# Performance work log

Measured on AMD Instinct MI355X. Metric: run time of the kernel, lower is better.

The kernel has to match this reference:

```python
import jax, jax.numpy as jnp
import numpy as np

SCALE = 1.0 / (100.0 ** 0.5)  # module hard-codes QK / sqrt(100)


def setup_inputs() -> dict:
    key = jax.random.key(0)
    k1, k2, k3 = jax.random.split(key, 3)
    B, S, D = 8, 2048, 512
    head_size = 64
    x = jax.random.normal(k1, (B, S, D), dtype=jnp.float32)
    kernel = jax.random.normal(k2, (3, D, head_size), dtype=jnp.float32) * 0.02
    dense = jax.random.normal(k3, (D, D), dtype=jnp.float32) * 0.02
    return {"x": x, "kernel": kernel, "dense": dense, "heads": 8}


def reference(x, kernel, dense, heads):
    # All heads use the SAME kernel slices in the original loop, so each
    # iteration produces an identical V; compute once and tile.
    WQ = jnp.einsum('bsd,dh->bsh', x, kernel[0])  # [B,S,Hd]
    WK = jnp.einsum('bsd,dh->bsh', x, kernel[1])
    WV = jnp.einsum('bsd,dh->bsh', x, kernel[2])
    scores = jnp.einsum('bqh,bkh->bqk', WQ, WK) * SCALE  # [B,S,S]
    attn = jax.nn.softmax(scores, axis=-1)
    V = jnp.einsum('bqk,bkh->bqh', attn, WV)  # [B,S,Hd]
    out = jnp.tile(V, (1, 1, heads))  # concat of identical heads -> [B,S,heads*Hd]
    return jnp.einsum('bsf,fo->bso', out, dense)
```

## Files before the change

### kernel.cpp

```cpp
#include <hip/hip_runtime.h>
#include <math.h>


typedef __bf16 bf16;
typedef __bf16 bf16x4v __attribute__((ext_vector_type(4)));
typedef __bf16 bf16x8v __attribute__((ext_vector_type(8)));
typedef float f32x4 __attribute__((ext_vector_type(4)));

namespace {
constexpr int kS = 2048;
constexpr int kD = 512;
constexpr int kH = 64;
constexpr int kRows = 16384;
}

#define MFMA16(a, b, c) __builtin_amdgcn_mfma_f32_16x16x32_bf16((a), (b), (c), 0, 0, 0)

__global__ __launch_bounds__(256) void prep_kernel(const float* __restrict__ w,
                                                   const float* __restrict__ dense,
                                                   bf16* __restrict__ wtg,
                                                   float* __restrict__ dr) {
  int idx = blockIdx.x * 256 + threadIdx.x;
  if (idx < 98304) {
    int mat = idx >> 15, rem = idx & 32767;
    int n = rem >> 9, k = rem & 511;
    wtg[idx] = (bf16)w[mat * 32768 + k * 64 + n];
  } else {
    int e = idx - 98304;
    int j = e >> 9, o = e & 511;
    float s = 0.f;
#pragma unroll
    for (int h = 0; h < 8; ++h) s += dense[(size_t)(h * 64 + j) * kD + o];
    dr[e] = s;
  }
}

__global__ __launch_bounds__(256) void proj_kernel(const float* __restrict__ x,
                                                   const bf16* __restrict__ wtg,
                                                   bf16* __restrict__ wq,
                                                   bf16* __restrict__ wk,
                                                   bf16* __restrict__ wvt) {
  const int bt = blockIdx.x;
  const int tid = threadIdx.x;
  const int w = tid >> 6, tx = tid & 15, quad = (tid >> 4) & 3;
  const int row0 = bt * 64;

  __shared__ bf16 Xs[64 * 72];
  __shared__ bf16 Wts[3 * 64 * 72];

  f32x4 acc[3][4];
#pragma unroll
  for (int m = 0; m < 3; ++m)
#pragma unroll
    for (int nt = 0; nt < 4; ++nt) acc[m][nt] = (f32x4){0.f, 0.f, 0.f, 0.f};

  for (int k0 = 0; k0 < kD; k0 += 64) {
    __syncthreads();
#pragma unroll
    for (int p = 0; p < 4; ++p) {
      int i4 = tid + p * 256;
      int r = i4 >> 4, c4 = (i4 & 15) * 4;
      float4 f = *(const float4*)&x[(size_t)(row0 + r) * kD + k0 + c4];
      bf16x4v h = {(bf16)f.x, (bf16)f.y, (bf16)f.z, (bf16)f.w};
      *(bf16x4v*)&Xs[r * 72 + c4] = h;
    }
#pragma unroll
    for (int p = 0; p < 6; ++p) {
      int cc = tid + p * 256;
      int mat = cc >> 9, rem = cc & 511;
      int n = rem >> 3, c8 = (rem & 7) * 8;
      *(uint4*)&Wts[(mat * 64 + n) * 72 + c8] =
          *(const uint4*)&wtg[(size_t)mat * 32768 + (size_t)n * 512 + k0 + c8];
    }
    __syncthreads();
#pragma unroll
    for (int s = 0; s < 2; ++s) {
      bf16x8v a = *(bf16x8v*)&Xs[(w * 16 + tx) * 72 + s * 32 + quad * 8];
#pragma unroll
      for (int m = 0; m < 3; ++m)
#pragma unroll
        for (int nt = 0; nt < 4; ++nt) {
          bf16x8v bfr =
              *(bf16x8v*)&Wts[(m * 64 + nt * 16 + tx) * 72 + s * 32 + quad * 8];
          acc[m][nt] = MFMA16(a, bfr, acc[m][nt]);
        }
    }
  }

#pragma unroll
  for (int nt = 0; nt < 4; ++nt)
#pragma unroll
    for (int r = 0; r < 4; ++r) {
      int row_g = row0 + w * 16 + quad * 4 + r;
      int col = nt * 16 + tx;
      wq[(size_t)row_g * 64 + col] = (bf16)acc[0][nt][r];
      wk[(size_t)row_g * 64 + col] = (bf16)acc[1][nt][r];
    }
  __syncthreads();
  bf16* Vt = Xs;
#pragma unroll
  for (int nt = 0; nt < 4; ++nt)
#pragma unroll
    for (int r = 0; r < 4; ++r)
      Vt[(nt * 16 + tx) * 72 + (w * 16 + quad * 4 + r)] = (bf16)acc[2][nt][r];
  __syncthreads();
#pragma unroll
  for (int p = 0; p < 2; ++p) {
    int c = tid + p * 256;
    int v = c >> 3, seg = c & 7;
    *(uint4*)&wvt[(size_t)v * kRows + row0 + seg * 8] =
        *(uint4*)&Vt[v * 72 + seg * 8];
  }
}

__global__ __launch_bounds__(512, 4) void flash_kernel(
    const bf16* __restrict__ wq, const bf16* __restrict__ wk,
    const bf16* __restrict__ wvt, float* __restrict__ vo) {
  const int bid = blockIdx.x;
  const int b = bid & 7, qb = bid >> 3;
  const int q0 = qb * 32;
  const int tid = threadIdx.x;
  const int w = tid >> 6, lane = tid & 63, tx = tid & 15, quad = (tid >> 4) & 3;

  __shared__ __align__(16) char lds[65536];
  __shared__ float Lsh[256];
  bf16* Ksw = (bf16*)(lds + w * 8192);
  bf16* Psw = Ksw;
  bf16* Vtw = (bf16*)(lds + w * 8192 + 4096);

  const bf16* wqb = wq + (size_t)(b * kS) * 64;
  const bf16* wkb = wk + (size_t)(b * kS) * 64;
  const bf16* wvb = wvt + b * kS;

  const int kc0 = (quad ^ (tx & 7)) * 8;
  const int kc1 = ((4 + quad) ^ (tx & 7)) * 8;
  const int h2 = (tx ^ (tx >> 2)) & 3;

  bf16x8v aq[2][2];
#pragma unroll
  for (int rt = 0; rt < 2; ++rt)
#pragma unroll
    for (int s = 0; s < 2; ++s)
      aq[rt][s] = *(const bf16x8v*)&wqb[(size_t)(q0 + rt * 16 + tx) * 64 +
                                        s * 32 + quad * 8];

  f32x4 oacc[2][4];
#pragma unroll
  for (int rt = 0; rt < 2; ++rt)
#pragma unroll
    for (int nt = 0; nt < 4; ++nt) oacc[rt][nt] = (f32x4){0.f, 0.f, 0.f, 0.f};
  float lsum[2][4] = {};

  const int ksr = lane >> 3, kslc = lane & 7;
  const int vsv = lane >> 2, vsck = lane & 3;

  for (int t = 0; t < 8; ++t) {
    const int k0 = (t * 8 + w) * 32;
#pragma unroll
    for (int j = 0; j < 4; ++j) {
      int r = ksr + j * 8;
      *(uint4*)&Ksw[r * 64 + ((kslc ^ (r & 7)) * 8)] =
          *(const uint4*)&wkb[(size_t)(k0 + r) * 64 + kslc * 8];
      int v = vsv + j * 16;
      *(uint4*)&Vtw[v * 32 + ((vsck ^ ((v ^ (v >> 2)) & 3)) * 8)] =
          *(const uint4*)&wvb[(size_t)v * kRows + k0 + vsck * 8];
    }

#pragma unroll
    for (int nt = 0; nt < 2; ++nt) {
      int krow = nt * 16 + tx;
      bf16x8v b0 = *(bf16x8v*)&Ksw[krow * 64 + kc0];
      bf16x8v b1 = *(bf16x8v*)&Ksw[krow * 64 + kc1];
#pragma unroll
      for (int rt = 0; rt < 2; ++rt) {
        f32x4 z = (f32x4){0.f, 0.f, 0.f, 0.f};
        z = MFMA16(aq[rt][0], b0, z);
        z = MFMA16(aq[rt][1], b1, z);
#pragma unroll
        for (int r = 0; r < 4; ++r) {
          float p = __expf(z[r] * 0.1f);
          lsum[rt][r] += p;
          int q = rt * 16 + quad * 4 + r;
          int chunk = nt * 2 + (tx >> 3);
          Psw[q * 32 + ((chunk ^ (r ^ quad)) * 8) + (tx & 7)] = (bf16)p;
        }
      }
    }

#pragma unroll
    for (int rt = 0; rt < 2; ++rt) {
      bf16x8v pa = *(bf16x8v*)&Psw[(rt * 16 + tx) * 32 + ((quad ^ h2) * 8)];
#pragma unroll
      for (int nt = 0; nt < 4; ++nt) {
        bf16x8v vb = *(bf16x8v*)&Vtw[(nt * 16 + tx) * 32 + ((quad ^ h2) * 8)];
        oacc[rt][nt] = MFMA16(pa, vb, oacc[rt][nt]);
      }
    }
  }

  __syncthreads();
  float* myO = (float*)(lds + w * 8192);
  float* myL = Lsh + w * 32;
#pragma unroll
  for (int rt = 0; rt < 2; ++rt)
#pragma unroll
    for (int nt = 0; nt < 4; ++nt)
#pragma unroll
      for (int r = 0; r < 4; ++r)
        myO[(rt * 16 + quad * 4 + r) * 64 + nt * 16 + tx] = oacc[rt][nt][r];
#pragma unroll
  for (int rt = 0; rt < 2; ++rt)
#pragma unroll
    for (int r = 0; r < 4; ++r) {
      float v = lsum[rt][r];
#pragma unroll
      for (int m = 1; m < 16; m <<= 1) v += __shfl_xor(v, m, 64);
      if (tx == 0) myL[rt * 16 + quad * 4 + r] = v;
    }
  __syncthreads();

#pragma unroll
  for (int p = 0; p < 4; ++p) {
    int e = tid + p * 512;
    int row = e >> 6;
    float s = 0.f, lt = 0.f;
#pragma unroll
    for (int wv = 0; wv < 8; ++wv) {
      s += ((const float*)(lds + wv * 8192))[e];
      lt += Lsh[wv * 32 + row];
    }
    vo[(size_t)(b * kS + q0 + row) * 64 + (e & 63)] = s / lt;
  }
}

__global__ __launch_bounds__(256) void out_gemm_kernel(
    const float* __restrict__ v, const float* __restrict__ dr,
    float* __restrict__ out) {
  const int rt = blockIdx.x, ct = blockIdx.y;
  const int tid = threadIdx.x;
  const int tx = tid & 15, ty = tid >> 4;

  __shared__ float As[64][68];
  __shared__ float Bs[64][68];

#pragma unroll
  for (int p = 0; p < 4; ++p) {
    int f4 = tid + p * 256;
    int r = f4 >> 4, c = (f4 & 15) * 4;
    *(float4*)&As[r][c] = *(const float4*)(v + (size_t)(rt * 64 + r) * kH + c);
    *(float4*)&Bs[r][c] = *(const float4*)(dr + (size_t)r * kD + ct * 64 + c);
  }
  __syncthreads();

  float acc[4][4] = {};
#pragma unroll
  for (int k = 0; k < 64; k += 4) {
    float a[4][4], bb[4][4];
#pragma unroll
    for (int i = 0; i < 4; ++i) {
      float4 t = *(const float4*)&As[ty * 4 + i][k];
      a[i][0] = t.x; a[i][1] = t.y; a[i][2] = t.z; a[i][3] = t.w;
    }
#pragma unroll
    for (int kk = 0; kk < 4; ++kk) {
      float4 t = *(const float4*)&Bs[k + kk][tx * 4];
      bb[kk][0] = t.x; bb[kk][1] = t.y; bb[kk][2] = t.z; bb[kk][3] = t.w;
    }
#pragma unroll
    for (int i = 0; i < 4; ++i)
#pragma unroll
      for (int kk = 0; kk < 4; ++kk)
#pragma unroll
        for (int j = 0; j < 4; ++j)
          acc[i][j] = fmaf(a[i][kk], bb[kk][j], acc[i][j]);
  }
#pragma unroll
  for (int i = 0; i < 4; ++i) {
    float4 vv = make_float4(acc[i][0], acc[i][1], acc[i][2], acc[i][3]);
    *(float4*)(out + (size_t)(rt * 64 + ty * 4 + i) * kD + ct * 64 + tx * 4) = vv;
  }
}

extern "C" void kernel_launch(void* const* d_in, const int* in_sizes, int n_in,
                              void* d_out, int out_size, void* d_ws,
                              size_t ws_size, hipStream_t stream) {
  const float* x = (const float*)d_in[0];
  const float* w = (const float*)d_in[1];
  const float* dense = (const float*)d_in[2];
  float* out = (float*)d_out;

  bf16* wq = (bf16*)d_ws;
  bf16* wk = wq + (size_t)kRows * 64;
  bf16* wvt = wk + (size_t)kRows * 64;
  bf16* wtg = wvt + (size_t)kRows * 64;
  float* dr = (float*)(wtg + 98304);
  float* vo = dr + 32768;

  prep_kernel<<<512, 256, 0, stream>>>(w, dense, wtg, dr);
  proj_kernel<<<256, 256, 0, stream>>>(x, wtg, wq, wk, wvt);
  flash_kernel<<<512, 512, 0, stream>>>(wq, wk, wvt, vo);
  out_gemm_kernel<<<dim3(kRows / 64, kD / 64), 256, 0, stream>>>(vo, dr, out);
}
```

Baseline: 142.5 us.

## Fuse output dense projection into flash attention epilogue with bf16 MFMA

The separate fp32 output GEMM kernel is removed. Its work now runs in the flash kernel epilogue: the normalized attention output is staged as bf16 in swizzled LDS and multiplied against a transposed bf16 head-summed dense matrix using MFMA. This avoids writing and re-reading the intermediate V output and drops one kernel launch. In exchange the epilogue adds bf16 rounding of V and of the dense weights, and extra LDS and global traffic inside the flash kernel, which can raise its register and LDS pressure.

```diff
diff --git a/kernel.cpp b/kernel.cpp
--- a/kernel.cpp
+++ b/kernel.cpp
@@ -10,7 +10,6 @@
 namespace {
 constexpr int kS = 2048;
 constexpr int kD = 512;
-constexpr int kH = 64;
 constexpr int kRows = 16384;
 }
 
@@ -19,7 +18,7 @@
 __global__ __launch_bounds__(256) void prep_kernel(const float* __restrict__ w,
                                                    const float* __restrict__ dense,
                                                    bf16* __restrict__ wtg,
-                                                   float* __restrict__ dr) {
+                                                   bf16* __restrict__ drt) {
   int idx = blockIdx.x * 256 + threadIdx.x;
   if (idx < 98304) {
     int mat = idx >> 15, rem = idx & 32767;
@@ -27,11 +26,11 @@
     wtg[idx] = (bf16)w[mat * 32768 + k * 64 + n];
   } else {
     int e = idx - 98304;
-    int j = e >> 9, o = e & 511;
+    int o = e >> 6, j = e & 63;
     float s = 0.f;
 #pragma unroll
     for (int h = 0; h < 8; ++h) s += dense[(size_t)(h * 64 + j) * kD + o];
-    dr[e] = s;
+    drt[e] = (bf16)s;
   }
 }
 
@@ -115,7 +114,8 @@
 
 __global__ __launch_bounds__(512, 4) void flash_kernel(
     const bf16* __restrict__ wq, const bf16* __restrict__ wk,
-    const bf16* __restrict__ wvt, float* __restrict__ vo) {
+    const bf16* __restrict__ wvt, const bf16* __restrict__ drt,
+    float* __restrict__ out) {
   const int bid = blockIdx.x;
   const int b = bid & 7, qb = bid >> 3;
   const int q0 = qb * 32;
@@ -124,6 +124,7 @@
 
   __shared__ __align__(16) char lds[65536];
   __shared__ float Lsh[256];
+  __shared__ __align__(16) bf16 vob[32 * 64];
   bf16* Ksw = (bf16*)(lds + w * 8192);
   bf16* Psw = Ksw;
   bf16* Vtw = (bf16*)(lds + w * 8192 + 4096);
@@ -222,62 +223,53 @@
 #pragma unroll
   for (int p = 0; p < 4; ++p) {
     int e = tid + p * 512;
-    int row = e >> 6;
+    int row = e >> 6, col = e & 63;
     float s = 0.f, lt = 0.f;
 #pragma unroll
     for (int wv = 0; wv < 8; ++wv) {
       s += ((const float*)(lds + wv * 8192))[e];
       lt += Lsh[wv * 32 + row];
     }
-    vo[(size_t)(b * kS + q0 + row) * 64 + (e & 63)] = s / lt;
-  }
-}
-
-__global__ __launch_bounds__(256) void out_gemm_kernel(
-    const float* __restrict__ v, const float* __restrict__ dr,
-    float* __restrict__ out) {
-  const int rt = blockIdx.x, ct = blockIdx.y;
-  const int tid = threadIdx.x;
-  const int tx = tid & 15, ty = tid >> 4;
-
-  __shared__ float As[64][68];
-  __shared__ float Bs[64][68];
-
-#pragma unroll
-  for (int p = 0; p < 4; ++p) {
-    int f4 = tid + p * 256;
-    int r = f4 >> 4, c = (f4 & 15) * 4;
-    *(float4*)&As[r][c] = *(const float4*)(v + (size_t)(rt * 64 + r) * kH + c);
-    *(float4*)&Bs[r][c] = *(const float4*)(dr + (size_t)r * kD + ct * 64 + c);
-  }
-  __syncthreads();
-
-  float acc[4][4] = {};
-#pragma unroll
-  for (int k = 0; k < 64; k += 4) {
-    float a[4][4], bb[4][4];
-#pragma unroll
-    for (int i = 0; i < 4; ++i) {
-      float4 t = *(const float4*)&As[ty * 4 + i][k];
-      a[i][0] = t.x; a[i][1] = t.y; a[i][2] = t.z; a[i][3] = t.w;
-    }
-#pragma unroll
-    for (int kk = 0; kk < 4; ++kk) {
-      float4 t = *(const float4*)&Bs[k + kk][tx * 4];
-      bb[kk][0] = t.x; bb[kk][1] = t.y; bb[kk][2] = t.z; bb[kk][3] = t.w;
-    }
-#pragma unroll
-    for (int i = 0; i < 4; ++i)
-#pragma unroll
-      for (int kk = 0; kk < 4; ++kk)
-#pragma unroll
-        for (int j = 0; j < 4; ++j)
-          acc[i][j] = fmaf(a[i][kk], bb[kk][j], acc[i][j]);
-  }
-#pragma unroll
-  for (int i = 0; i < 4; ++i) {
-    float4 vv = make_float4(acc[i][0], acc[i][1], acc[i][2], acc[i][3]);
-    *(float4*)(out + (size_t)(rt * 64 + ty * 4 + i) * kD + ct * 64 + tx * 4) = vv;
+    vob[row * 64 + (((col >> 3) ^ (row & 7)) * 8) + (col & 7)] = (bf16)(s / lt);
+  }
+  __syncthreads();
+
+  bf16x8v av[2][2];
+#pragma unroll
+  for (int rt = 0; rt < 2; ++rt) {
+    av[rt][0] = *(bf16x8v*)&vob[(rt * 16 + tx) * 64 + kc0];
+    av[rt][1] = *(bf16x8v*)&vob[(rt * 16 + tx) * 64 + kc1];
+  }
+
+  float* OutS = (float*)lds;
+#pragma unroll
+  for (int c = 0; c < 2; ++c) {
+    if (c) __syncthreads();
+#pragma unroll
+    for (int i = 0; i < 2; ++i) {
+      const int ct = c * 16 + w * 2 + i;
+      bf16x8v bd0 =
+          *(const bf16x8v*)&drt[(size_t)(ct * 16 + tx) * 64 + quad * 8];
+      bf16x8v bd1 =
+          *(const bf16x8v*)&drt[(size_t)(ct * 16 + tx) * 64 + 32 + quad * 8];
+#pragma unroll
+      for (int rt = 0; rt < 2; ++rt) {
+        f32x4 z = (f32x4){0.f, 0.f, 0.f, 0.f};
+        z = MFMA16(av[rt][0], bd0, z);
+        z = MFMA16(av[rt][1], bd1, z);
+#pragma unroll
+        for (int r = 0; r < 4; ++r)
+          OutS[(rt * 16 + quad * 4 + r) * 260 + (w * 2 + i) * 16 + tx] = z[r];
+      }
+    }
+    __syncthreads();
+#pragma unroll
+    for (int p = 0; p < 4; ++p) {
+      int e = tid + p * 512;
+      int row = e >> 6, seg = e & 63;
+      *(float4*)&out[(size_t)(b * kS + q0 + row) * kD + c * 256 + seg * 4] =
+          *(float4*)&OutS[row * 260 + seg * 4];
+    }
   }
 }
 
@@ -293,11 +285,9 @@
   bf16* wk = wq + (size_t)kRows * 64;
   bf16* wvt = wk + (size_t)kRows * 64;
   bf16* wtg = wvt + (size_t)kRows * 64;
-  float* dr = (float*)(wtg + 98304);
-  float* vo = dr + 32768;
-
-  prep_kernel<<<512, 256, 0, stream>>>(w, dense, wtg, dr);
+  bf16* drt = wtg + 98304;
+
+  prep_kernel<<<512, 256, 0, stream>>>(w, dense, wtg, drt);
   proj_kernel<<<256, 256, 0, stream>>>(x, wtg, wq, wk, wvt);
-  flash_kernel<<<512, 512, 0, stream>>>(wq, wk, wvt, vo);
-  out_gemm_kernel<<<dim3(kRows / 64, kD / 64), 256, 0, stream>>>(vo, dr, out);
-}
+  flash_kernel<<<512, 512, 0, stream>>>(wq, wk, wvt, drt, out);
+}
```

New measurement: 138.4 us (median of 2 runs). -2.9%, faster.
